# Kernel tuning notes

Hardware: AMD Instinct MI355X
Metric: run time of the kernel (lower is better)

## Reference

```python
import jax, jax.numpy as jnp
import numpy as np
from jax import lax

B, C, H, L = 4, 64, 8, 2048  # batch, per-head channels, heads, sequence length


def setup_inputs() -> dict:
    key = jax.random.key(0)
    ks = jax.random.split(key, 15)

    def p(k, shape, s=0.05):
        return jax.random.normal(k, shape, jnp.float32) * s

    inp = {"x": jax.random.normal(ks[0], (B, C, L), jnp.float32)}
    for i, nm in enumerate(["q", "k", "v"]):
        inp[f"{nm}_dw"] = p(ks[1 + 4 * i], (C, 1, 3))       # depthwise conv weight, groups=C, k=3
        inp[f"{nm}_db"] = p(ks[2 + 4 * i], (C,))
        inp[f"{nm}_pw"] = p(ks[3 + 4 * i], (H * C, C))      # pointwise 1x1 conv weight
        inp[f"{nm}_pb"] = p(ks[4 + 4 * i], (H * C,))
    inp["u_w"] = p(ks[13], (C, H * C))                      # unify_heads 1x1 conv weight
    inp["u_b"] = p(ks[14], (C,))
    return inp


def dsconv(x, dw, db, pw, pb):
    # Depth-separable conv1d: depthwise (k=3, pad=1, groups=C) then pointwise 1x1.
    c = x.shape[1]
    y = lax.conv_general_dilated(x, dw, window_strides=(1,), padding=[(1, 1)],
                                 dimension_numbers=("NCH", "OIH", "NCH"),
                                 feature_group_count=c)
    y = y + db[None, :, None]
    return jnp.einsum("bcl,oc->bol", y, pw) + pb[None, :, None]


def reference(x, q_dw, q_db, q_pw, q_pb, k_dw, k_db, k_pw, k_pb,
              v_dw, v_db, v_pw, v_pb, u_w, u_b):
    b, c, l = x.shape
    h = H
    scale = c ** (-0.25)
    q = dsconv(x, q_dw, q_db, q_pw, q_pb).reshape(b, h, c, l) * scale
    k = dsconv(x, k_dw, k_db, k_pw, k_pb).reshape(b, h, c, l) * scale
    v = dsconv(x, v_dw, v_db, v_pw, v_pb).reshape(b, h, c, l)
    # dot[b,h,i,j] = sum_c k[b,h,c,i] * q[b,h,c,j]  (i = key pos, j = query pos)
    dot = jnp.einsum("bhci,bhcj->bhij", k, q)
    att = jax.nn.softmax(dot, axis=2)  # normalize over key positions (torch dim=1 of [bh,l,l])
    out = jnp.einsum("bhci,bhij->bhcj", v, att).reshape(b, h * c, l)
    return jnp.einsum("bkl,ck->bcl", out, u_w) + u_b[None, :, None]
```

## Files before the change

kernel.cpp:

```cpp
#include <hip/hip_runtime.h>
#include <hip/hip_bf16.h>
#include <stdint.h>
#include <string.h>

typedef unsigned short u16;
typedef unsigned int u32;
typedef __bf16 bf16x8 __attribute__((ext_vector_type(8)));
typedef float f32x4 __attribute__((ext_vector_type(4)));
typedef unsigned int u32x2v __attribute__((ext_vector_type(2)));

#define NB 4
#define NC 64
#define NH 8
#define NL 2048
#define HC 512

#define XT_OFF  ((size_t)0)
#define WM_OFF  ((size_t)1 << 20)
#define PBM_OFF ((size_t)2 << 20)
#define V_OFF   ((size_t)4 << 20)
#define QT_OFF  ((size_t)12 << 20)
#define KT_OFF  ((size_t)20 << 20)

#define LP 68

#if __has_builtin(__builtin_amdgcn_exp2f)
#define EXP2F __builtin_amdgcn_exp2f
#else
#define EXP2F exp2f
#endif

static __device__ __forceinline__ u16 f2bfu(float f) {
  union { float f; unsigned int i; } x; x.f = f;
  unsigned int i = x.i;
  return (u16)((i + 0x7fffu + ((i >> 16) & 1u)) >> 16);
}
static __device__ __forceinline__ u32 pk2(float a, float b) {
  float2 f; f.x = a; f.y = b;
  __hip_bfloat162 h = __float22bfloat162_rn(f);
  u32 w; __builtin_memcpy(&w, &h, 4); return w;
}
static __device__ __forceinline__ bf16x8 ld_bf8(const u16* p) {
  bf16x8 v; __builtin_memcpy(&v, p, 16); return v;
}
static __device__ __forceinline__ bf16x8 frag_from4(u32 a, u32 b, u32 c, u32 d) {
  u32 t[4] = {a, b, c, d};
  bf16x8 v; __builtin_memcpy(&v, t, 16); return v;
}

#define XCHG(X_, Y_, Fa_, Fb_)                                              \
  {                                                                         \
    u32x2v a_ = __builtin_amdgcn_permlane32_swap((X_), (Y_), false, false); \
    u32x2v b_ = __builtin_amdgcn_permlane16_swap(a_.x, a_.y, false, false); \
    Fa_ = b_.x; Fb_ = b_.y;                                                 \
  }

__global__ __launch_bounds__(256) void prep_all(
    const float* __restrict__ x,
    const float* __restrict__ qdw, const float* __restrict__ qdb,
    const float* __restrict__ qpw, const float* __restrict__ qpb,
    const float* __restrict__ kdw, const float* __restrict__ kdb,
    const float* __restrict__ kpw, const float* __restrict__ kpb,
    const float* __restrict__ vdw, const float* __restrict__ vdb,
    const float* __restrict__ vpw, const float* __restrict__ vpb,
    const float* __restrict__ ub,
    u16* __restrict__ Wm, float* __restrict__ pbm,
    u16* __restrict__ xT, float* __restrict__ out)
{
  __shared__ __align__(16) u16 T[64 * LP];
  int bx = blockIdx.x;
  int tid = threadIdx.x;

  if (bx < 512) {
    int i4 = bx * 256 + tid;
    int c = (i4 >> 9) & 63;
    float f = ub[c];
    float4 v = {f, f, f, f};
    ((float4*)out)[i4] = v;
    return;
  }
  if (bx < 902) {
    int idx = (bx - 512) * 256 + tid;
    if (idx < 98304) {
      int tns = idx >> 15, r = idx & 32767, o = r >> 6, c = r & 63;
      const float* dw = (tns == 0) ? qdw : (tns == 1) ? kdw : vdw;
      const float* pw = (tns == 0) ? qpw : (tns == 1) ? kpw : vpw;
      float s = (tns == 0) ? 0.35355339059327373f * 1.4426950408889634f
              : (tns == 1) ? 0.35355339059327373f : 1.0f;
      float w = pw[o * 64 + c] * s;
#pragma unroll
      for (int d = 0; d < 3; ++d)
        Wm[((size_t)(tns * 3 + d) * 512 + o) * 64 + c] = f2bfu(w * dw[c * 3 + d]);
    } else {
      int i = idx - 98304;
      int tns = i >> 9, o = i & 511;
      const float* db = (tns == 0) ? qdb : (tns == 1) ? kdb : vdb;
      const float* pw = (tns == 0) ? qpw : (tns == 1) ? kpw : vpw;
      const float* pb = (tns == 0) ? qpb : (tns == 1) ? kpb : vpb;
      float s = (tns == 0) ? 0.35355339059327373f * 1.4426950408889634f
              : (tns == 1) ? 0.35355339059327373f : 1.0f;
      float bias = pb[o];
      for (int c = 0; c < 64; ++c) bias += pw[o * 64 + c] * db[c];
      pbm[i] = bias * s;
    }
    return;
  }
  {
    int b2 = bx - 902;
    int lt = b2 & 31, b = b2 >> 5;
    {
      int c = tid & 63, ls = (tid >> 6) * 16;
      const float4* g = (const float4*)(x + ((size_t)b * NC + c) * NL + lt * 64 + ls);
      u16 tmp[16];
#pragma unroll
      for (int j4 = 0; j4 < 4; ++j4) {
        float4 f = g[j4];
        tmp[j4*4+0] = f2bfu(f.x); tmp[j4*4+1] = f2bfu(f.y);
        tmp[j4*4+2] = f2bfu(f.z); tmp[j4*4+3] = f2bfu(f.w);
      }
#pragma unroll
      for (int j = 0; j < 16; ++j) T[(ls + j) * LP + c] = tmp[j];
    }
    __syncthreads();
    {
      int r = tid >> 2, cs = (tid & 3) * 16;
      uint4 a = *(const uint4*)&T[r * LP + cs];
      uint4 b3 = *(const uint4*)&T[r * LP + cs + 8];
      u16* o = xT + ((size_t)b * NL + lt * 64 + r) * 64 + cs;
      *(uint4*)o = a;
      *(uint4*)(o + 8) = b3;
    }
  }
}

__global__ __launch_bounds__(256) void qkv_gemm(
    const u16* __restrict__ xT, const u16* __restrict__ Wm,
    const float* __restrict__ pbm,
    u16* __restrict__ v, u16* __restrict__ qT, u16* __restrict__ kT)
{
  __shared__ __align__(16) u16 WS[3][64 * LP];
  __shared__ __align__(16) u16 XS[2][66 * LP];
  __shared__ __align__(16) u16 OS[64 * LP];

  int bx = blockIdx.x;
  int lg  = bx & 7;
  int och = (bx >> 3) & 7;
  int tmp = bx >> 6;
  int tns = tmp % 3;
  int b   = tmp / 3;

  int tid = threadIdx.x;
  int wave = tid >> 6, lane = tid & 63, quad = lane >> 4, l16 = lane & 15;
  const u16* xg = xT + (size_t)b * NL * 64;

  {
    const u16* wg = Wm + ((size_t)(tns * 3) * 512 + och * 64) * 64;
#pragma unroll
    for (int it = 0; it < 6; ++it) {
      int s = tid + it * 256;
      int d = s >> 9, r = s & 511;
      int o = r >> 3, c4 = r & 7;
      uint4 w = *(const uint4*)(wg + ((size_t)d * 512 + o) * 64 + c4 * 8);
      *(uint4*)&WS[d][o * LP + c4 * 8] = w;
    }
  }

  int xr0 = tid >> 3,          xc0 = (tid & 7) * 8;
  int xr1 = (tid + 256) >> 3,  xc1 = xc0;
  int xr2 = (tid + 512) >> 3,  xc2 = xc0;
  uint4 R0, R1, R2;
  uint4 Z = {0, 0, 0, 0};

#define LOAD_XS(tt)                                                         \
  {                                                                         \
    int base = (lg * 4 + (tt)) * 64 - 1;                                    \
    int g0 = base + xr0, g1 = base + xr1, g2 = base + xr2;                  \
    R0 = ((unsigned)g0 < NL) ? *(const uint4*)(xg + (size_t)g0 * 64 + xc0) : Z; \
    R1 = ((unsigned)g1 < NL) ? *(const uint4*)(xg + (size_t)g1 * 64 + xc1) : Z; \
    if (tid < 16)                                                           \
      R2 = ((unsigned)g2 < NL) ? *(const uint4*)(xg + (size_t)g2 * 64 + xc2) : Z; \
  }
#define STORE_XS(bf)                                                        \
  {                                                                         \
    *(uint4*)&XS[bf][xr0 * LP + xc0] = R0;                                  \
    *(uint4*)&XS[bf][xr1 * LP + xc1] = R1;                                  \
    if (tid < 16) *(uint4*)&XS[bf][xr2 * LP + xc2] = R2;                    \
  }

  LOAD_XS(0); STORE_XS(0);
  LOAD_XS(1);
  __syncthreads();

  float bias4[4];
  bf16x8 aw[3][2];
  if (tns == 2) {
    const float* pbt = pbm + tns * 512 + och * 64 + wave * 16;
#pragma unroll
    for (int rr = 0; rr < 4; ++rr) bias4[rr] = pbt[quad * 4 + rr];
#pragma unroll
    for (int d = 0; d < 3; ++d)
#pragma unroll
      for (int kh = 0; kh < 2; ++kh)
        aw[d][kh] = ld_bf8(&WS[d][(wave * 16 + l16) * LP + kh * 32 + quad * 8]);
  } else {
    const float* pbt = pbm + tns * 512 + och * 64;
#pragma unroll
    for (int nt = 0; nt < 4; ++nt) bias4[nt] = pbt[nt * 16 + l16];
  }

  for (int t = 0; t < 4; ++t) {
    int cur = t & 1;
    f32x4 acc[4] = {{0,0,0,0},{0,0,0,0},{0,0,0,0},{0,0,0,0}};

    if (tns == 2) {
#pragma unroll
      for (int nt = 0; nt < 4; ++nt)
#pragma unroll
        for (int d = 0; d < 3; ++d)
#pragma unroll
          for (int kh = 0; kh < 2; ++kh) {
            bf16x8 bx8 = ld_bf8(&XS[cur][(nt * 16 + l16 + d) * LP + kh * 32 + quad * 8]);
            acc[nt] = __builtin_amdgcn_mfma_f32_16x16x32_bf16(aw[d][kh], bx8, acc[nt], 0, 0, 0);
          }
    } else {
      bf16x8 ax[3][2];
#pragma unroll
      for (int d = 0; d < 3; ++d)
#pragma unroll
        for (int kh = 0; kh < 2; ++kh)
          ax[d][kh] = ld_bf8(&XS[cur][(wave * 16 + l16 + d) * LP + kh * 32 + quad * 8]);
#pragma unroll
      for (int nt = 0; nt < 4; ++nt)
#pragma unroll
        for (int d = 0; d < 3; ++d)
#pragma unroll
          for (int kh = 0; kh < 2; ++kh) {
            bf16x8 bw = ld_bf8(&WS[d][(nt * 16 + l16) * LP + kh * 32 + quad * 8]);
            acc[nt] = __builtin_amdgcn_mfma_f32_16x16x32_bf16(ax[d][kh], bw, acc[nt], 0, 0, 0);
          }
    }

    if (t < 3) { STORE_XS((t + 1) & 1); if (t < 2) LOAD_XS(t + 2); }
    __syncthreads();

    if (tns == 2) {
#pragma unroll
      for (int nt = 0; nt < 4; ++nt)
#pragma unroll
        for (int rr = 0; rr < 4; ++rr)
          OS[(wave * 16 + quad * 4 + rr) * LP + nt * 16 + l16] =
              f2bfu(acc[nt][rr] + bias4[rr]);
    } else {
#pragma unroll
      for (int nt = 0; nt < 4; ++nt)
#pragma unroll
        for (int rr = 0; rr < 4; ++rr)
          OS[(wave * 16 + quad * 4 + rr) * LP + nt * 16 + l16] =
              f2bfu(acc[nt][rr] + bias4[nt]);
    }
    __syncthreads();

    {
      int lt = lg * 4 + t;
      int r = tid >> 2, ck = (tid & 3) * 16;
      uint4 a = *(const uint4*)&OS[r * LP + ck];
      uint4 b2 = *(const uint4*)&OS[r * LP + ck + 8];
      u16* gp;
      if (tns == 2)
        gp = v + ((size_t)(b * HC + och * 64 + r)) * NL + lt * 64 + ck;
      else {
        u16* dst = (tns == 0) ? qT : kT;
        gp = dst + ((size_t)(b * 8 + och) * NL + lt * 64 + r) * 64 + ck;
      }
      *(uint4*)gp = a;
      *(uint4*)(gp + 8) = b2;
    }
  }
#undef LOAD_XS
#undef STORE_XS
}

__global__ __launch_bounds__(512, 4) void attn_kernel(
    const u16* __restrict__ qT, const u16* __restrict__ kT,
    const u16* __restrict__ vg, const float* __restrict__ uw,
    float* __restrict__ outg)
{
  __shared__ __align__(16) u16 Kt[2][64 * LP];
  __shared__ __align__(16) u16 Vt[2][64 * LP];
  __shared__ __align__(16) u16 UW[64 * LP];

  int bx = blockIdx.x;
  int qt = bx & 15, bh = bx >> 4;
  int b = bh >> 3, h = bh & 7;
  int tid = threadIdx.x;
  int wave = tid >> 6, lane = tid & 63, quad = lane >> 4, l16 = lane & 15;

  const u16* Qh = qT + (size_t)bh * NL * 64;
  const u16* Kh = kT + (size_t)bh * NL * 64;
  const u16* Vh = vg + ((size_t)(b * HC + h * NC)) * NL;
  int q0 = qt * 128;

  int sr = tid >> 3, ss = (tid & 7) * 8;
  int vc = tid >> 3, vk = (tid & 7) * 8;

  {
    int c = tid >> 3, g = (tid & 7) * 8;
    const float4* s = (const float4*)(uw + (size_t)c * HC + h * 64 + g);
    float4 w0 = s[0], w1 = s[1];
    u16* d = &UW[c * LP + g];
    d[0] = f2bfu(w0.x); d[1] = f2bfu(w0.y); d[2] = f2bfu(w0.z); d[3] = f2bfu(w0.w);
    d[4] = f2bfu(w1.x); d[5] = f2bfu(w1.y); d[6] = f2bfu(w1.z); d[7] = f2bfu(w1.w);
  }

  uint4 ka, va;
  {
    ka = *(const uint4*)(Kh + (size_t)sr * 64 + ss);
    va = *(const uint4*)(Vh + (size_t)vc * NL + vk);
    *(uint4*)&Kt[0][sr * LP + ss] = ka;
    *(uint4*)&Vt[0][vc * LP + vk] = va;
    ka = *(const uint4*)(Kh + (size_t)(64 + sr) * 64 + ss);
    va = *(const uint4*)(Vh + (size_t)vc * NL + 64 + vk);
  }

  bf16x8 bq[2];
#pragma unroll
  for (int kh = 0; kh < 2; ++kh)
    bq[kh] = ld_bf8(Qh + (size_t)(q0 + wave * 16 + l16) * 64 + kh * 32 + quad * 8);

  __syncthreads();

  f32x4 o[4];
#pragma unroll
  for (int ct = 0; ct < 4; ++ct) o[ct] = (f32x4){0, 0, 0, 0};
  float l_part = 0.f;

  for (int i = 0; i < 32; ++i) {
    int cur = i & 1;
    bf16x8 ak[4][2], av[4][2];
#pragma unroll
    for (int j = 0; j < 4; ++j)
#pragma unroll
      for (int kh = 0; kh < 2; ++kh) {
        ak[j][kh] = ld_bf8(&Kt[cur][(j * 16 + l16) * LP + kh * 32 + quad * 8]);
        av[j][kh] = ld_bf8(&Vt[cur][(j * 16 + l16) * LP + kh * 32 + quad * 8]);
      }

    f32x4 s[4];
#pragma unroll
    for (int ktl = 0; ktl < 4; ++ktl) {
      f32x4 z = {0, 0, 0, 0};
      z = __builtin_amdgcn_mfma_f32_16x16x32_bf16(ak[ktl][0], bq[0], z, 0, 0, 0);
      z = __builtin_amdgcn_mfma_f32_16x16x32_bf16(ak[ktl][1], bq[1], z, 0, 0, 0);
      s[ktl] = z;
    }
    u32 w01[4], w23[4];
#pragma unroll
    for (int ktl = 0; ktl < 4; ++ktl) {
      float p0 = EXP2F(s[ktl][0]);
      float p1 = EXP2F(s[ktl][1]);
      float p2 = EXP2F(s[ktl][2]);
      float p3 = EXP2F(s[ktl][3]);
      l_part += (p0 + p1) + (p2 + p3);
      w01[ktl] = pk2(p0, p1);
      w23[ktl] = pk2(p2, p3);
    }
#pragma unroll
    for (int kh = 0; kh < 2; ++kh) {
      u32 F0, F1, F2, F3;
      XCHG(w01[2 * kh], w01[2 * kh + 1], F0, F2);
      XCHG(w23[2 * kh], w23[2 * kh + 1], F1, F3);
      bf16x8 bp = frag_from4(F0, F1, F2, F3);
#pragma unroll
      for (int ct = 0; ct < 4; ++ct)
        o[ct] = __builtin_amdgcn_mfma_f32_16x16x32_bf16(av[ct][kh], bp, o[ct], 0, 0, 0);
    }

    if (i < 31) {
      int nxt = cur ^ 1;
      *(uint4*)&Kt[nxt][sr * LP + ss] = ka;
      *(uint4*)&Vt[nxt][vc * LP + vk] = va;
      if (i < 30) {
        int kt2 = (i + 2) * 64;
        ka = *(const uint4*)(Kh + (size_t)(kt2 + sr) * 64 + ss);
        va = *(const uint4*)(Vh + (size_t)vc * NL + kt2 + vk);
      }
    }
    __syncthreads();
  }

  float* ob = outg + ((size_t)b * NC) * NL;
  {
    float lp = l_part;
    lp += __shfl_xor(lp, 16);
    lp += __shfl_xor(lp, 32);
    float rinv = 1.0f / lp;

    u32 w01[4], w23[4];
#pragma unroll
    for (int ct = 0; ct < 4; ++ct) {
      w01[ct] = pk2(o[ct][0] * rinv, o[ct][1] * rinv);
      w23[ct] = pk2(o[ct][2] * rinv, o[ct][3] * rinv);
    }
    bf16x8 ot[2];
#pragma unroll
    for (int kh = 0; kh < 2; ++kh) {
      u32 F0, F1, F2, F3;
      XCHG(w01[2 * kh], w01[2 * kh + 1], F0, F2);
      XCHG(w23[2 * kh], w23[2 * kh + 1], F1, F3);
      ot[kh] = frag_from4(F0, F1, F2, F3);
    }

    int qcol = q0 + wave * 16 + l16;
#pragma unroll
    for (int mt = 0; mt < 4; ++mt) {
      f32x4 acc = {0, 0, 0, 0};
#pragma unroll
      for (int kh = 0; kh < 2; ++kh) {
        bf16x8 a = ld_bf8(&UW[(mt * 16 + l16) * LP + kh * 32 + quad * 8]);
        acc = __builtin_amdgcn_mfma_f32_16x16x32_bf16(a, ot[kh], acc, 0, 0, 0);
      }
#pragma unroll
      for (int rr = 0; rr < 4; ++rr) {
        int c = mt * 16 + quad * 4 + rr;
        atomicAdd(&ob[(size_t)c * NL + qcol], acc[rr]);
      }
    }
  }
}

extern "C" void kernel_launch(void* const* d_in, const int* in_sizes, int n_in,
                              void* d_out, int out_size, void* d_ws, size_t ws_size,
                              hipStream_t stream) {
  (void)in_sizes; (void)n_in; (void)out_size; (void)ws_size;
  const float* x   = (const float*)d_in[0];
  const float* qdw = (const float*)d_in[1];
  const float* qdb = (const float*)d_in[2];
  const float* qpw = (const float*)d_in[3];
  const float* qpb = (const float*)d_in[4];
  const float* kdw = (const float*)d_in[5];
  const float* kdb = (const float*)d_in[6];
  const float* kpw = (const float*)d_in[7];
  const float* kpb = (const float*)d_in[8];
  const float* vdw = (const float*)d_in[9];
  const float* vdb = (const float*)d_in[10];
  const float* vpw = (const float*)d_in[11];
  const float* vpb = (const float*)d_in[12];
  const float* uw  = (const float*)d_in[13];
  const float* ub  = (const float*)d_in[14];

  char* ws = (char*)d_ws;
  u16*   xT  = (u16*)(ws + XT_OFF);
  u16*   Wm  = (u16*)(ws + WM_OFF);
  float* pbm = (float*)(ws + PBM_OFF);
  u16*   v   = (u16*)(ws + V_OFF);
  u16*   qT  = (u16*)(ws + QT_OFF);
  u16*   kT  = (u16*)(ws + KT_OFF);
  float* out = (float*)d_out;

  prep_all<<<1030, 256, 0, stream>>>(
      x, qdw, qdb, qpw, qpb, kdw, kdb, kpw, kpb, vdw, vdb, vpw, vpb,
      ub, Wm, pbm, xT, out);
  qkv_gemm<<<768, 256, 0, stream>>>(xT, Wm, pbm, v, qT, kT);
  attn_kernel<<<512, 512, 0, stream>>>(qT, kT, v, uw, out);
}
```

Measured before the change: 153.7 us.

## Split key tile across wave pairs so each wave reuses K/V fragments for two query tiles

Each wave now owns 32 queries, as two 16-query tiles, and half of each 64-key tile. The two waves that share a query group exchange their softmax denominators through LDS and both atomically add their partial projected outputs. This halves the per-wave LDS fragment reads of K and V by reusing them across two query tiles. In exchange it doubles the number of global atomicAdds into the output and adds an LDS reduction plus an extra barrier in the epilogue.

Result: slower. 160.5 us (+4.5%).

```diff
diff --git a/kernel.cpp b/kernel.cpp
--- a/kernel.cpp
+++ b/kernel.cpp
@@ -288,12 +288,14 @@
   __shared__ __align__(16) u16 Kt[2][64 * LP];
   __shared__ __align__(16) u16 Vt[2][64 * LP];
   __shared__ __align__(16) u16 UW[64 * LP];
+  __shared__ float LX[8][2][16];
 
   int bx = blockIdx.x;
   int qt = bx & 15, bh = bx >> 4;
   int b = bh >> 3, h = bh & 7;
   int tid = threadIdx.x;
   int wave = tid >> 6, lane = tid & 63, quad = lane >> 4, l16 = lane & 15;
+  int qs = wave >> 1, kb = wave & 1;
 
   const u16* Qh = qT + (size_t)bh * NL * 64;
   const u16* Kh = kT + (size_t)bh * NL * 64;
@@ -322,57 +324,54 @@
     va = *(const uint4*)(Vh + (size_t)vc * NL + 64 + vk);
   }
 
-  bf16x8 bq[2];
-#pragma unroll
-  for (int kh = 0; kh < 2; ++kh)
-    bq[kh] = ld_bf8(Qh + (size_t)(q0 + wave * 16 + l16) * 64 + kh * 32 + quad * 8);
+  bf16x8 bq[2][2];
+#pragma unroll
+  for (int t = 0; t < 2; ++t)
+#pragma unroll
+    for (int kh = 0; kh < 2; ++kh)
+      bq[t][kh] = ld_bf8(Qh + (size_t)(q0 + qs * 32 + t * 16 + l16) * 64 +
+                         kh * 32 + quad * 8);
 
   __syncthreads();
 
-  f32x4 o[4];
-#pragma unroll
-  for (int ct = 0; ct < 4; ++ct) o[ct] = (f32x4){0, 0, 0, 0};
-  float l_part = 0.f;
+  f32x4 o[2][4];
+#pragma unroll
+  for (int t = 0; t < 2; ++t)
+#pragma unroll
+    for (int ct = 0; ct < 4; ++ct) o[t][ct] = (f32x4){0, 0, 0, 0};
+  float l_part[2] = {0.f, 0.f};
 
   for (int i = 0; i < 32; ++i) {
     int cur = i & 1;
-    bf16x8 ak[4][2], av[4][2];
-#pragma unroll
-    for (int j = 0; j < 4; ++j)
-#pragma unroll
-      for (int kh = 0; kh < 2; ++kh) {
-        ak[j][kh] = ld_bf8(&Kt[cur][(j * 16 + l16) * LP + kh * 32 + quad * 8]);
-        av[j][kh] = ld_bf8(&Vt[cur][(j * 16 + l16) * LP + kh * 32 + quad * 8]);
-      }
-
-    f32x4 s[4];
-#pragma unroll
-    for (int ktl = 0; ktl < 4; ++ktl) {
-      f32x4 z = {0, 0, 0, 0};
-      z = __builtin_amdgcn_mfma_f32_16x16x32_bf16(ak[ktl][0], bq[0], z, 0, 0, 0);
-      z = __builtin_amdgcn_mfma_f32_16x16x32_bf16(ak[ktl][1], bq[1], z, 0, 0, 0);
-      s[ktl] = z;
-    }
-    u32 w01[4], w23[4];
-#pragma unroll
-    for (int ktl = 0; ktl < 4; ++ktl) {
-      float p0 = EXP2F(s[ktl][0]);
-      float p1 = EXP2F(s[ktl][1]);
-      float p2 = EXP2F(s[ktl][2]);
-      float p3 = EXP2F(s[ktl][3]);
-      l_part += (p0 + p1) + (p2 + p3);
-      w01[ktl] = pk2(p0, p1);
-      w23[ktl] = pk2(p2, p3);
-    }
-#pragma unroll
-    for (int kh = 0; kh < 2; ++kh) {
+    bf16x8 ak[2][2], av[4];
+#pragma unroll
+    for (int j = 0; j < 2; ++j)
+#pragma unroll
+      for (int ch = 0; ch < 2; ++ch)
+        ak[j][ch] = ld_bf8(&Kt[cur][(kb * 32 + j * 16 + l16) * LP + ch * 32 + quad * 8]);
+#pragma unroll
+    for (int ct = 0; ct < 4; ++ct)
+      av[ct] = ld_bf8(&Vt[cur][(ct * 16 + l16) * LP + kb * 32 + quad * 8]);
+
+#pragma unroll
+    for (int t = 0; t < 2; ++t) {
+      f32x4 s0 = {0, 0, 0, 0}, s1 = {0, 0, 0, 0};
+      s0 = __builtin_amdgcn_mfma_f32_16x16x32_bf16(ak[0][0], bq[t][0], s0, 0, 0, 0);
+      s0 = __builtin_amdgcn_mfma_f32_16x16x32_bf16(ak[0][1], bq[t][1], s0, 0, 0, 0);
+      s1 = __builtin_amdgcn_mfma_f32_16x16x32_bf16(ak[1][0], bq[t][0], s1, 0, 0, 0);
+      s1 = __builtin_amdgcn_mfma_f32_16x16x32_bf16(ak[1][1], bq[t][1], s1, 0, 0, 0);
+      float p0 = EXP2F(s0[0]), p1 = EXP2F(s0[1]), p2 = EXP2F(s0[2]), p3 = EXP2F(s0[3]);
+      float p4 = EXP2F(s1[0]), p5 = EXP2F(s1[1]), p6 = EXP2F(s1[2]), p7 = EXP2F(s1[3]);
+      l_part[t] += ((p0 + p1) + (p2 + p3)) + ((p4 + p5) + (p6 + p7));
+      u32 wA0 = pk2(p0, p1), wB0 = pk2(p2, p3);
+      u32 wA1 = pk2(p4, p5), wB1 = pk2(p6, p7);
       u32 F0, F1, F2, F3;
-      XCHG(w01[2 * kh], w01[2 * kh + 1], F0, F2);
-      XCHG(w23[2 * kh], w23[2 * kh + 1], F1, F3);
+      XCHG(wA0, wA1, F0, F2);
+      XCHG(wB0, wB1, F1, F3);
       bf16x8 bp = frag_from4(F0, F1, F2, F3);
 #pragma unroll
       for (int ct = 0; ct < 4; ++ct)
-        o[ct] = __builtin_amdgcn_mfma_f32_16x16x32_bf16(av[ct][kh], bp, o[ct], 0, 0, 0);
+        o[t][ct] = __builtin_amdgcn_mfma_f32_16x16x32_bf16(av[ct], bp, o[t][ct], 0, 0, 0);
     }
 
     if (i < 31) {
@@ -388,18 +387,29 @@
     __syncthreads();
   }
 
-  float* ob = outg + ((size_t)b * NC) * NL;
-  {
-    float lp = l_part;
+#pragma unroll
+  for (int t = 0; t < 2; ++t) {
+    float lp = l_part[t];
     lp += __shfl_xor(lp, 16);
     lp += __shfl_xor(lp, 32);
-    float rinv = 1.0f / lp;
+    l_part[t] = lp;
+  }
+  if (quad == 0) {
+    LX[wave][0][l16] = l_part[0];
+    LX[wave][1][l16] = l_part[1];
+  }
+  __syncthreads();
+
+  float* ob = outg + ((size_t)b * NC) * NL;
+#pragma unroll
+  for (int t = 0; t < 2; ++t) {
+    float rinv = 1.0f / (LX[wave][t][l16] + LX[wave ^ 1][t][l16]);
 
     u32 w01[4], w23[4];
 #pragma unroll
     for (int ct = 0; ct < 4; ++ct) {
-      w01[ct] = pk2(o[ct][0] * rinv, o[ct][1] * rinv);
-      w23[ct] = pk2(o[ct][2] * rinv, o[ct][3] * rinv);
+      w01[ct] = pk2(o[t][ct][0] * rinv, o[t][ct][1] * rinv);
+      w23[ct] = pk2(o[t][ct][2] * rinv, o[t][ct][3] * rinv);
     }
     bf16x8 ot[2];
 #pragma unroll
@@ -410,7 +420,7 @@
       ot[kh] = frag_from4(F0, F1, F2, F3);
     }
 
-    int qcol = q0 + wave * 16 + l16;
+    int qcol = q0 + qs * 32 + t * 16 + l16;
 #pragma unroll
     for (int mt = 0; mt < 4; ++mt) {
       f32x4 acc = {0, 0, 0, 0};
```

## Halve attention block size, single-buffer K/V, compute row sums via MFMA

Applied to the files above, without the earlier changes.

The attention kernel now runs 1024 blocks of 256 threads, each covering 64 query columns instead of 128, so more blocks can spread across CUs. K/V shared tiles go from double- to single-buffered, with an extra barrier before each overwrite, and each thread loads twice as much per tile. The softmax denominator is now accumulated with an MFMA against a ones fragment, replacing scalar adds and cross-lane shuffles. The trade-off is more total K/V traffic (each tile is loaded by twice as many blocks) and less overlap from losing the double buffer.

Measured after the change: 158.2 us. 1.03x slower.

```diff
diff --git a/kernel.cpp b/kernel.cpp
--- a/kernel.cpp
+++ b/kernel.cpp
@@ -280,17 +280,17 @@
 #undef STORE_XS
 }
 
-__global__ __launch_bounds__(512, 4) void attn_kernel(
+__global__ __launch_bounds__(256, 4) void attn_kernel(
     const u16* __restrict__ qT, const u16* __restrict__ kT,
     const u16* __restrict__ vg, const float* __restrict__ uw,
     float* __restrict__ outg)
 {
-  __shared__ __align__(16) u16 Kt[2][64 * LP];
-  __shared__ __align__(16) u16 Vt[2][64 * LP];
+  __shared__ __align__(16) u16 Kt[64 * LP];
+  __shared__ __align__(16) u16 Vt[64 * LP];
   __shared__ __align__(16) u16 UW[64 * LP];
 
   int bx = blockIdx.x;
-  int qt = bx & 15, bh = bx >> 4;
+  int qt = bx & 31, bh = bx >> 5;
   int b = bh >> 3, h = bh & 7;
   int tid = threadIdx.x;
   int wave = tid >> 6, lane = tid & 63, quad = lane >> 4, l16 = lane & 15;
@@ -298,28 +298,36 @@
   const u16* Qh = qT + (size_t)bh * NL * 64;
   const u16* Kh = kT + (size_t)bh * NL * 64;
   const u16* Vh = vg + ((size_t)(b * HC + h * NC)) * NL;
-  int q0 = qt * 128;
-
-  int sr = tid >> 3, ss = (tid & 7) * 8;
-  int vc = tid >> 3, vk = (tid & 7) * 8;
+  int q0 = qt * 64;
+
+  int sr = tid >> 2, ss = (tid & 3) * 16;
+  int vc = tid >> 2, vk = (tid & 3) * 16;
 
   {
-    int c = tid >> 3, g = (tid & 7) * 8;
+    int c = tid >> 2, g = (tid & 3) * 16;
     const float4* s = (const float4*)(uw + (size_t)c * HC + h * 64 + g);
-    float4 w0 = s[0], w1 = s[1];
-    u16* d = &UW[c * LP + g];
-    d[0] = f2bfu(w0.x); d[1] = f2bfu(w0.y); d[2] = f2bfu(w0.z); d[3] = f2bfu(w0.w);
-    d[4] = f2bfu(w1.x); d[5] = f2bfu(w1.y); d[6] = f2bfu(w1.z); d[7] = f2bfu(w1.w);
-  }
-
-  uint4 ka, va;
+#pragma unroll
+    for (int j = 0; j < 4; ++j) {
+      float4 w = s[j];
+      u16* d = &UW[c * LP + g + j * 4];
+      d[0] = f2bfu(w.x); d[1] = f2bfu(w.y); d[2] = f2bfu(w.z); d[3] = f2bfu(w.w);
+    }
+  }
+
+  uint4 ka, kb, va, vb;
   {
-    ka = *(const uint4*)(Kh + (size_t)sr * 64 + ss);
-    va = *(const uint4*)(Vh + (size_t)vc * NL + vk);
-    *(uint4*)&Kt[0][sr * LP + ss] = ka;
-    *(uint4*)&Vt[0][vc * LP + vk] = va;
-    ka = *(const uint4*)(Kh + (size_t)(64 + sr) * 64 + ss);
-    va = *(const uint4*)(Vh + (size_t)vc * NL + 64 + vk);
+    const u16* ks = Kh + (size_t)sr * 64 + ss;
+    ka = *(const uint4*)ks; kb = *(const uint4*)(ks + 8);
+    const u16* vs = Vh + (size_t)vc * NL + vk;
+    va = *(const uint4*)vs; vb = *(const uint4*)(vs + 8);
+    *(uint4*)&Kt[sr * LP + ss] = ka;
+    *(uint4*)&Kt[sr * LP + ss + 8] = kb;
+    *(uint4*)&Vt[vc * LP + vk] = va;
+    *(uint4*)&Vt[vc * LP + vk + 8] = vb;
+    const u16* ks1 = Kh + (size_t)(64 + sr) * 64 + ss;
+    ka = *(const uint4*)ks1; kb = *(const uint4*)(ks1 + 8);
+    const u16* vs1 = Vh + (size_t)vc * NL + 64 + vk;
+    va = *(const uint4*)vs1; vb = *(const uint4*)(vs1 + 8);
   }
 
   bf16x8 bq[2];
@@ -327,22 +335,23 @@
   for (int kh = 0; kh < 2; ++kh)
     bq[kh] = ld_bf8(Qh + (size_t)(q0 + wave * 16 + l16) * 64 + kh * 32 + quad * 8);
 
+  bf16x8 ones = frag_from4(0x3F803F80u, 0x3F803F80u, 0x3F803F80u, 0x3F803F80u);
+
   __syncthreads();
 
   f32x4 o[4];
 #pragma unroll
   for (int ct = 0; ct < 4; ++ct) o[ct] = (f32x4){0, 0, 0, 0};
-  float l_part = 0.f;
+  f32x4 lacc = {0, 0, 0, 0};
 
   for (int i = 0; i < 32; ++i) {
-    int cur = i & 1;
     bf16x8 ak[4][2], av[4][2];
 #pragma unroll
     for (int j = 0; j < 4; ++j)
 #pragma unroll
       for (int kh = 0; kh < 2; ++kh) {
-        ak[j][kh] = ld_bf8(&Kt[cur][(j * 16 + l16) * LP + kh * 32 + quad * 8]);
-        av[j][kh] = ld_bf8(&Vt[cur][(j * 16 + l16) * LP + kh * 32 + quad * 8]);
+        ak[j][kh] = ld_bf8(&Kt[(j * 16 + l16) * LP + kh * 32 + quad * 8]);
+        av[j][kh] = ld_bf8(&Vt[(j * 16 + l16) * LP + kh * 32 + quad * 8]);
       }
 
     f32x4 s[4];
@@ -360,7 +369,6 @@
       float p1 = EXP2F(s[ktl][1]);
       float p2 = EXP2F(s[ktl][2]);
       float p3 = EXP2F(s[ktl][3]);
-      l_part += (p0 + p1) + (p2 + p3);
       w01[ktl] = pk2(p0, p1);
       w23[ktl] = pk2(p2, p3);
     }
@@ -370,19 +378,24 @@
       XCHG(w01[2 * kh], w01[2 * kh + 1], F0, F2);
       XCHG(w23[2 * kh], w23[2 * kh + 1], F1, F3);
       bf16x8 bp = frag_from4(F0, F1, F2, F3);
+      lacc = __builtin_amdgcn_mfma_f32_16x16x32_bf16(ones, bp, lacc, 0, 0, 0);
 #pragma unroll
       for (int ct = 0; ct < 4; ++ct)
         o[ct] = __builtin_amdgcn_mfma_f32_16x16x32_bf16(av[ct][kh], bp, o[ct], 0, 0, 0);
     }
 
+    __syncthreads();
     if (i < 31) {
-      int nxt = cur ^ 1;
-      *(uint4*)&Kt[nxt][sr * LP + ss] = ka;
-      *(uint4*)&Vt[nxt][vc * LP + vk] = va;
+      *(uint4*)&Kt[sr * LP + ss] = ka;
+      *(uint4*)&Kt[sr * LP + ss + 8] = kb;
+      *(uint4*)&Vt[vc * LP + vk] = va;
+      *(uint4*)&Vt[vc * LP + vk + 8] = vb;
       if (i < 30) {
         int kt2 = (i + 2) * 64;
-        ka = *(const uint4*)(Kh + (size_t)(kt2 + sr) * 64 + ss);
-        va = *(const uint4*)(Vh + (size_t)vc * NL + kt2 + vk);
+        const u16* ks = Kh + (size_t)(kt2 + sr) * 64 + ss;
+        ka = *(const uint4*)ks; kb = *(const uint4*)(ks + 8);
+        const u16* vs = Vh + (size_t)vc * NL + kt2 + vk;
+        va = *(const uint4*)vs; vb = *(const uint4*)(vs + 8);
       }
     }
     __syncthreads();
@@ -390,10 +403,7 @@
 
   float* ob = outg + ((size_t)b * NC) * NL;
   {
-    float lp = l_part;
-    lp += __shfl_xor(lp, 16);
-    lp += __shfl_xor(lp, 32);
-    float rinv = 1.0f / lp;
+    float rinv = 1.0f / lacc[0];
 
     u32 w01[4], w23[4];
 #pragma unroll
@@ -461,5 +471,5 @@
       x, qdw, qdb, qpw, qpb, kdw, kdb, kpw, kpb, vdw, vdb, vpw, vpb,
       ub, Wm, pbm, xT, out);
   qkv_gemm<<<768, 256, 0, stream>>>(xT, Wm, pbm, v, qT, kT);
-  attn_kernel<<<512, 512, 0, stream>>>(qT, kT, v, uw, out);
-}
+  attn_kernel<<<1024, 256, 0, stream>>>(qT, kT, v, uw, out);
+}
```
